# Kernel tuning notes

Hardware: AMD Instinct MI355X
Metric: run time of the kernel (lower is better)

## Reference

```python
import jax, jax.numpy as jnp
import numpy as np

NUM_EXPERTS = 32
TOP_K = 4
HIDDEN = 1024
FFN = 2048
BATCH, SEQ = 1, 1024


def setup_inputs() -> dict:
    key = jax.random.key(0)
    ks = jax.random.split(key, 4)
    s = 0.02
    return {
        "x": jax.random.normal(ks[0], (BATCH, SEQ, HIDDEN), jnp.float32),
        "gate_w": jax.random.normal(ks[1], (HIDDEN, NUM_EXPERTS), jnp.float32) * s,
        "gate_b": jnp.zeros((NUM_EXPERTS,), jnp.float32),
        "w1": jax.random.normal(ks[2], (NUM_EXPERTS, HIDDEN, FFN), jnp.float32) * s,
        "b1": jnp.zeros((NUM_EXPERTS, FFN), jnp.float32),
        "w2": jax.random.normal(ks[3], (NUM_EXPERTS, FFN, HIDDEN), jnp.float32) * s,
        "b2": jnp.zeros((NUM_EXPERTS, HIDDEN), jnp.float32),
        "load_ema": jnp.ones((NUM_EXPERTS,), jnp.float32) / NUM_EXPERTS,
        "top_k": TOP_K,
    }


def reference(x, gate_w, gate_b, w1, b1, w2, b2, load_ema, top_k):
    # x: [B, S, d]; eval-mode CompoundMoELayer forward.
    B, S, d = x.shape
    E = gate_w.shape[1]
    flat = x.reshape(-1, d)                              # [N, d]
    N = flat.shape[0]

    # --- router: gate logits -> top-k -> softmax over selected logits ---
    logits = flat @ gate_w + gate_b                      # [N, E]
    top_vals, top_idx = jax.lax.top_k(logits, top_k)     # [N, k]
    weights = jax.nn.softmax(top_vals, axis=-1)          # [N, k]

    # --- switch-style load-balance aux loss ---
    probs = jax.nn.softmax(logits, axis=-1)              # [N, E]
    counts = jax.nn.one_hot(top_idx, E, dtype=flat.dtype).sum(axis=1)  # [N, E]
    frac = counts.mean(axis=0) / top_k                   # [E] routed fraction
    base_aux = E * jnp.sum(frac * probs.mean(axis=0))

    # --- dense combine weights [N, E]: zero for non-selected experts ---
    comb = jnp.zeros((N, E), flat.dtype).at[jnp.arange(N)[:, None], top_idx].add(weights)

    # --- per-expert FFN (GELU, exact erf as torch default), combined ---
    def step(acc, p):
        W1, bb1, W2, bb2, ce = p                         # ce: [N] combine weight
        h = jax.nn.gelu(flat @ W1 + bb1, approximate=False)
        y = h @ W2 + bb2
        return acc + ce[:, None] * y, None

    out, _ = jax.lax.scan(step, jnp.zeros_like(flat), (w1, b1, w2, b2, comb.T))

    # --- compound entropy regularizer over expert load EMA buffer ---
    lp = load_ema / (load_ema.sum() + 1e-8)
    entropy = -jnp.sum(lp * jnp.log(lp + 1e-8))
    reg = jnp.log(jnp.asarray(E, flat.dtype)) - entropy
    aux = base_aux + 0.001 * reg
    return out.reshape(B, S, d), aux
```

## Files before the change

kernel.cpp:

```cpp
#include <hip/hip_runtime.h>
#include <hip/hip_bf16.h>
#include <cmath>

#define N_TOK 1024
#define DIM   1024
#define FFN   2048
#define NE    32
#define TOPK  4
#define TM    192
#define TN    64
#define BK    32
#define BS_STRIDE 40

typedef __attribute__((ext_vector_type(8))) short bf16x8;
typedef __attribute__((ext_vector_type(4))) float f32x4;

#define GLOBAL_AS __attribute__((address_space(1)))
#define LDS_AS    __attribute__((address_space(3)))

__device__ __forceinline__ void g2lds16(const void* g, void* l) {
    __builtin_amdgcn_global_load_lds((const GLOBAL_AS void*)g, (LDS_AS void*)l, 16, 0, 0);
}

__global__ __launch_bounds__(256) void router_kernel(
        const float* __restrict__ x, const float* __restrict__ gw,
        const float* __restrict__ gb, float* __restrict__ probs_mat,
        int* __restrict__ top_idx, float* __restrict__ top_w,
        __hip_bfloat16* __restrict__ xb) {
    __shared__ float part[8][32];
    __shared__ float logit_s[32];
    int t = threadIdx.x;
    int token = blockIdx.x;
    const float* xr = x + (size_t)token * DIM;
    {
        float4 v = *(const float4*)&xr[t * 4];
        union { __hip_bfloat16 h[4]; ushort4 u; } pk;
        pk.h[0] = __float2bfloat16(v.x); pk.h[1] = __float2bfloat16(v.y);
        pk.h[2] = __float2bfloat16(v.z); pk.h[3] = __float2bfloat16(v.w);
        *(ushort4*)&xb[(size_t)token * DIM + t * 4] = pk.u;
    }
    int e = t & 31, p = t >> 5;
    float acc = 0.f;
    int i0 = p * (DIM / 8);
    for (int i = 0; i < DIM / 8; ++i)
        acc += xr[i0 + i] * gw[(size_t)(i0 + i) * NE + e];
    part[p][e] = acc;
    __syncthreads();
    if (t < 64) {
        float l = -3e38f;
        if (t < 32) {
            l = gb[t];
            for (int q = 0; q < 8; ++q) l += part[q][t];
        }
        float m = l;
        for (int off = 32; off >= 1; off >>= 1) m = fmaxf(m, __shfl_xor(m, off, 64));
        float ex = (t < 32) ? expf(l - m) : 0.f;
        float den = ex;
        for (int off = 32; off >= 1; off >>= 1) den += __shfl_xor(den, off, 64);
        if (t < 32) probs_mat[(size_t)token * 32 + t] = ex / den;
        float v = l;
        float vals[TOPK]; int idxs[TOPK];
        for (int r = 0; r < TOPK; ++r) {
            float mv = v;
            for (int off = 32; off >= 1; off >>= 1) mv = fmaxf(mv, __shfl_xor(mv, off, 64));
            unsigned long long mask = __ballot(v == mv);
            int idx = __ffsll((unsigned long long)(mask & 0xffffffffull)) - 1;
            vals[r] = mv; idxs[r] = idx;
            if (t == idx) v = -3e38f;
        }
        if (t == 0) {
            float w[TOPK]; float ss = 0.f;
            for (int r = 0; r < TOPK; ++r) { w[r] = expf(vals[r] - vals[0]); ss += w[r]; }
            for (int r = 0; r < TOPK; ++r) {
                top_idx[token * TOPK + r] = idxs[r];
                top_w[token * TOPK + r] = w[r] / ss;
            }
        }
    }
}

__global__ void aux_kernel(const float* __restrict__ probs_mat, const int* __restrict__ top_idx,
                           const float* __restrict__ load_ema, int* __restrict__ offsets,
                           int* __restrict__ cursors, float* __restrict__ out_aux) {
    __shared__ int cnt_s[32];
    __shared__ float ps[32];
    __shared__ float psum_part[8][32];
    int t = threadIdx.x;
    if (t < 32) cnt_s[t] = 0;
    __syncthreads();
    for (int i = t; i < N_TOK * TOPK; i += 256) atomicAdd(&cnt_s[top_idx[i]], 1);
    int e = t & 31, p = t >> 5;
    float s = 0.f;
    for (int tok = p; tok < N_TOK; tok += 8) s += probs_mat[(size_t)tok * 32 + e];
    psum_part[p][e] = s;
    __syncthreads();
    if (t < 32) {
        float tot = 0.f;
        for (int q = 0; q < 8; ++q) tot += psum_part[q][t];
        ps[t] = tot;
    }
    __syncthreads();
    if (t == 0) {
        int off = 0;
        for (int i = 0; i < 32; ++i) { offsets[i] = off; cursors[i] = off; off += cnt_s[i]; }
        offsets[32] = off;
        float base = 0.f;
        for (int i = 0; i < 32; ++i) {
            float frac = (float)cnt_s[i] / (float)(N_TOK * TOPK);
            base += frac * (ps[i] / (float)N_TOK);
        }
        base *= (float)NE;
        float sum_ema = 0.f;
        for (int i = 0; i < 32; ++i) sum_ema += load_ema[i];
        float H = 0.f;
        for (int i = 0; i < 32; ++i) {
            float lp = load_ema[i] / (sum_ema + 1e-8f);
            H -= lp * logf(lp + 1e-8f);
        }
        *out_aux = base + 0.001f * (logf((float)NE) - H);
    }
}

__global__ void scatter_kernel(const int* __restrict__ top_idx, int* __restrict__ cursors,
                               int* __restrict__ pair_token, int* __restrict__ pair_of) {
    int token = blockIdx.x * 256 + threadIdx.x;
    if (token >= N_TOK) return;
    for (int s = 0; s < TOPK; ++s) {
        int e = top_idx[token * TOPK + s];
        int pos = atomicAdd(&cursors[e], 1);
        pair_token[pos] = token;
        pair_of[token * TOPK + s] = pos;
    }
}

__global__ __launch_bounds__(256, 4) void gemm1_kernel(
        const __hip_bfloat16* __restrict__ xb, const float* __restrict__ w1,
        const float* __restrict__ b1, const int* __restrict__ offsets,
        const int* __restrict__ pair_token, __hip_bfloat16* __restrict__ h) {
    int e = blockIdx.z;
    int m0 = offsets[e], Me = offsets[e + 1] - m0;
    int f0 = blockIdx.x * TN;

    __shared__ short As[4 * TM * 8];
    __shared__ __hip_bfloat16 Bs[TN * BS_STRIDE];
    __shared__ int toks[TM];

    int t = threadIdx.x;
    int w = t >> 6, ln = t & 63;
    int q = ln >> 4, lj = ln & 15;
    int bn = ln, bkb = w * 8;

    float bias[4];
#pragma unroll
    for (int ns = 0; ns < 4; ++ns) bias[ns] = b1[(size_t)e * FFN + f0 + ns * 16 + lj];

    for (int mb = 0; mb < Me; mb += TM) {
        int mlim = Me - mb; if (mlim > TM) mlim = TM;
        if (t < TM) {
            int r = t < mlim ? t : mlim - 1;
            toks[t] = pair_token[m0 + mb + r];
        }
        f32x4 acc[3][4] = {};
        for (int k0 = 0; k0 < DIM; k0 += BK) {
            __syncthreads();
#pragma unroll
            for (int c = 0; c < 3; ++c) {
                const __hip_bfloat16* src = xb + (size_t)toks[c * 64 + ln] * DIM + k0 + w * 8;
                g2lds16(src, As + (w * TM + c * 64) * 8);
            }
            {
                const float* bp = w1 + ((size_t)e * DIM + k0 + bkb) * FFN + f0 + bn;
                union { __hip_bfloat16 hb[8]; int4 v; } u;
#pragma unroll
                for (int j = 0; j < 8; ++j) u.hb[j] = __float2bfloat16(bp[(size_t)j * FFN]);
                *(int4*)&Bs[bn * BS_STRIDE + bkb] = u.v;
            }
            __syncthreads();
            bf16x8 af[3], bf[4];
#pragma unroll
            for (int ms = 0; ms < 3; ++ms)
                af[ms] = *(const bf16x8*)&As[(q * TM + w * 48 + ms * 16 + lj) * 8];
#pragma unroll
            for (int ns = 0; ns < 4; ++ns)
                bf[ns] = *(const bf16x8*)&Bs[(ns * 16 + lj) * BS_STRIDE + q * 8];
#pragma unroll
            for (int ms = 0; ms < 3; ++ms)
#pragma unroll
                for (int ns = 0; ns < 4; ++ns)
                    acc[ms][ns] = __builtin_amdgcn_mfma_f32_16x16x32_bf16(af[ms], bf[ns], acc[ms][ns], 0, 0, 0);
        }
#pragma unroll
        for (int ms = 0; ms < 3; ++ms) {
#pragma unroll
            for (int rr = 0; rr < 4; ++rr) {
                int rit = w * 48 + ms * 16 + q * 4 + rr;
                if (rit >= mlim) continue;
                size_t rowG = (size_t)(m0 + mb + rit);
#pragma unroll
                for (int ns = 0; ns < 4; ++ns) {
                    float v = acc[ms][ns][rr] + bias[ns];
                    float g = 0.5f * v * (1.f + erff(v * 0.70710678118654752f));
                    h[rowG * FFN + f0 + ns * 16 + lj] = __float2bfloat16(g);
                }
            }
        }
    }
}

__global__ __launch_bounds__(256, 4) void gemm2_kernel(
        const __hip_bfloat16* __restrict__ h, const float* __restrict__ w2,
        const int* __restrict__ offsets, float* __restrict__ y) {
    int e = blockIdx.z;
    int m0 = offsets[e], Me = offsets[e + 1] - m0;
    int d0 = blockIdx.x * TN;
    int kbase = blockIdx.y * (FFN / 2);
    float* yp = y + (size_t)blockIdx.y * N_TOK * TOPK * DIM;

    __shared__ short As[4 * TM * 8];
    __shared__ __hip_bfloat16 Bs[TN * BS_STRIDE];

    int t = threadIdx.x;
    int w = t >> 6, ln = t & 63;
    int q = ln >> 4, lj = ln & 15;
    int bn = ln, bkb = w * 8;

    for (int mb = 0; mb < Me; mb += TM) {
        int mlim = Me - mb; if (mlim > TM) mlim = TM;
        f32x4 acc[3][4] = {};
        for (int k0 = 0; k0 < FFN / 2; k0 += BK) {
            __syncthreads();
#pragma unroll
            for (int c = 0; c < 3; ++c) {
                int rit = c * 64 + ln;
                int r = rit < mlim ? rit : mlim - 1;
                const __hip_bfloat16* src = h + (size_t)(m0 + mb + r) * FFN + kbase + k0 + w * 8;
                g2lds16(src, As + (w * TM + c * 64) * 8);
            }
            {
                const float* bp = w2 + ((size_t)e * FFN + kbase + k0 + bkb) * DIM + d0 + bn;
                union { __hip_bfloat16 hb[8]; int4 v; } u;
#pragma unroll
                for (int j = 0; j < 8; ++j) u.hb[j] = __float2bfloat16(bp[(size_t)j * DIM]);
                *(int4*)&Bs[bn * BS_STRIDE + bkb] = u.v;
            }
            __syncthreads();
            bf16x8 af[3], bf[4];
#pragma unroll
            for (int ms = 0; ms < 3; ++ms)
                af[ms] = *(const bf16x8*)&As[(q * TM + w * 48 + ms * 16 + lj) * 8];
#pragma unroll
            for (int ns = 0; ns < 4; ++ns)
                bf[ns] = *(const bf16x8*)&Bs[(ns * 16 + lj) * BS_STRIDE + q * 8];
#pragma unroll
            for (int ms = 0; ms < 3; ++ms)
#pragma unroll
                for (int ns = 0; ns < 4; ++ns)
                    acc[ms][ns] = __builtin_amdgcn_mfma_f32_16x16x32_bf16(af[ms], bf[ns], acc[ms][ns], 0, 0, 0);
        }
#pragma unroll
        for (int ms = 0; ms < 3; ++ms) {
#pragma unroll
            for (int rr = 0; rr < 4; ++rr) {
                int rit = w * 48 + ms * 16 + q * 4 + rr;
                if (rit >= mlim) continue;
                size_t rowG = (size_t)(m0 + mb + rit);
#pragma unroll
                for (int ns = 0; ns < 4; ++ns)
                    yp[rowG * DIM + d0 + ns * 16 + lj] = acc[ms][ns][rr];
            }
        }
    }
}

__global__ void combine_kernel(const float* __restrict__ y, const float* __restrict__ b2,
        const int* __restrict__ top_idx, const float* __restrict__ top_w,
        const int* __restrict__ pair_of, float* __restrict__ out) {
    const float* y1 = y + (size_t)N_TOK * TOPK * DIM;
    int token = blockIdx.y;
    int j = blockIdx.x * 256 + threadIdx.x;
    float acc = 0.f;
#pragma unroll
    for (int s = 0; s < TOPK; ++s) {
        int e = top_idx[token * TOPK + s];
        float w = top_w[token * TOPK + s];
        int p = pair_of[token * TOPK + s];
        acc += w * (y[(size_t)p * DIM + j] + y1[(size_t)p * DIM + j] + b2[(size_t)e * DIM + j]);
    }
    out[(size_t)token * DIM + j] = acc;
}

extern "C" void kernel_launch(void* const* d_in, const int* in_sizes, int n_in,
                              void* d_out, int out_size, void* d_ws, size_t ws_size,
                              hipStream_t stream) {
    const float* x        = (const float*)d_in[0];
    const float* gate_w   = (const float*)d_in[1];
    const float* gate_b   = (const float*)d_in[2];
    const float* w1       = (const float*)d_in[3];
    const float* b1       = (const float*)d_in[4];
    const float* w2       = (const float*)d_in[5];
    const float* b2       = (const float*)d_in[6];
    const float* load_ema = (const float*)d_in[7];
    float* out = (float*)d_out;

    char* base = (char*)d_ws;
    size_t off = 0;
    auto alloc = [&](size_t bytes) {
        void* p = base + off;
        off = (off + bytes + 255) & ~(size_t)255;
        return p;
    };
    float* probs_mat = (float*)alloc(N_TOK * 32 * sizeof(float));
    int*   top_idx   = (int*)  alloc(N_TOK * TOPK * sizeof(int));
    float* top_w     = (float*)alloc(N_TOK * TOPK * sizeof(float));
    int*   offsets   = (int*)  alloc(33 * sizeof(int));
    int*   cursors   = (int*)  alloc(32 * sizeof(int));
    int*   pair_token= (int*)  alloc(N_TOK * TOPK * sizeof(int));
    int*   pair_of   = (int*)  alloc(N_TOK * TOPK * sizeof(int));
    __hip_bfloat16* xb = (__hip_bfloat16*)alloc((size_t)N_TOK * DIM * sizeof(__hip_bfloat16));
    __hip_bfloat16* h  = (__hip_bfloat16*)alloc((size_t)N_TOK * TOPK * FFN * sizeof(__hip_bfloat16));
    float* y         = (float*)alloc((size_t)2 * N_TOK * TOPK * DIM * sizeof(float));

    router_kernel<<<N_TOK, 256, 0, stream>>>(x, gate_w, gate_b, probs_mat, top_idx, top_w, xb);
    aux_kernel<<<1, 256, 0, stream>>>(probs_mat, top_idx, load_ema, offsets, cursors,
                                      out + (size_t)N_TOK * DIM);
    scatter_kernel<<<(N_TOK + 255) / 256, 256, 0, stream>>>(top_idx, cursors, pair_token, pair_of);
    {
        dim3 grid(FFN / TN, 1, NE);
        gemm1_kernel<<<grid, 256, 0, stream>>>(xb, w1, b1, offsets, pair_token, h);
    }
    {
        dim3 grid(DIM / TN, 2, NE);
        gemm2_kernel<<<grid, 256, 0, stream>>>(h, w2, offsets, y);
    }
    {
        dim3 grid(DIM / 256, N_TOK);
        combine_kernel<<<grid, 256, 0, stream>>>(y, b2, top_idx, top_w, pair_of, out);
    }
}
```

Baseline: 666.1 us.

## Double-buffer GEMM tiles and fuse weighted combine into gemm2 via atomics

Both expert GEMM kernels now double-buffer the LDS A/B tiles. The next K-slice's global loads and the bf16 conversion of the fp32 weights overlap the MFMA work on the current slice, and each iteration needs one barrier instead of two. The separate combine kernel and its large fp32 y intermediate are removed: gemm2 scales its partial results by the routing weight, adds the bias on the first K-half, and atomically accumulates straight into a pre-zeroed output. This cuts an 8M-float round trip through memory, at the cost of float atomic contention and an order-dependent, non-deterministic summation.

Result: no change. 676.4 us (+1.5%).

```diff
diff --git a/kernel.cpp b/kernel.cpp
--- a/kernel.cpp
+++ b/kernel.cpp
@@ -22,13 +22,16 @@
     __builtin_amdgcn_global_load_lds((const GLOBAL_AS void*)g, (LDS_AS void*)l, 16, 0, 0);
 }
 
+__global__ void zero_kernel(float4* __restrict__ p) {
+    p[blockIdx.x * 256 + threadIdx.x] = float4{0.f, 0.f, 0.f, 0.f};
+}
+
 __global__ __launch_bounds__(256) void router_kernel(
         const float* __restrict__ x, const float* __restrict__ gw,
         const float* __restrict__ gb, float* __restrict__ probs_mat,
         int* __restrict__ top_idx, float* __restrict__ top_w,
         __hip_bfloat16* __restrict__ xb) {
     __shared__ float part[8][32];
-    __shared__ float logit_s[32];
     int t = threadIdx.x;
     int token = blockIdx.x;
     const float* xr = x + (size_t)token * DIM;
@@ -121,15 +124,16 @@
     }
 }
 
-__global__ void scatter_kernel(const int* __restrict__ top_idx, int* __restrict__ cursors,
-                               int* __restrict__ pair_token, int* __restrict__ pair_of) {
+__global__ void scatter_kernel(const int* __restrict__ top_idx, const float* __restrict__ top_w,
+                               int* __restrict__ cursors,
+                               int* __restrict__ pair_token, float* __restrict__ pair_w) {
     int token = blockIdx.x * 256 + threadIdx.x;
     if (token >= N_TOK) return;
     for (int s = 0; s < TOPK; ++s) {
         int e = top_idx[token * TOPK + s];
         int pos = atomicAdd(&cursors[e], 1);
         pair_token[pos] = token;
-        pair_of[token * TOPK + s] = pos;
+        pair_w[pos] = top_w[token * TOPK + s];
     }
 }
 
@@ -139,10 +143,11 @@
         const int* __restrict__ pair_token, __hip_bfloat16* __restrict__ h) {
     int e = blockIdx.z;
     int m0 = offsets[e], Me = offsets[e + 1] - m0;
+    if (Me <= 0) return;
     int f0 = blockIdx.x * TN;
 
-    __shared__ short As[4 * TM * 8];
-    __shared__ __hip_bfloat16 Bs[TN * BS_STRIDE];
+    __shared__ __attribute__((aligned(16))) short As[2][4 * TM * 8];
+    __shared__ __attribute__((aligned(16))) __hip_bfloat16 Bs[2][TN * BS_STRIDE];
     __shared__ int toks[TM];
 
     int t = threadIdx.x;
@@ -154,40 +159,65 @@
 #pragma unroll
     for (int ns = 0; ns < 4; ++ns) bias[ns] = b1[(size_t)e * FFN + f0 + ns * 16 + lj];
 
+    const float* bbase = w1 + ((size_t)e * DIM + bkb) * FFN + f0 + bn;
+
     for (int mb = 0; mb < Me; mb += TM) {
         int mlim = Me - mb; if (mlim > TM) mlim = TM;
+        __syncthreads();
         if (t < TM) {
             int r = t < mlim ? t : mlim - 1;
             toks[t] = pair_token[m0 + mb + r];
         }
+        __syncthreads();
+
+        float br[8];
+#pragma unroll
+        for (int j = 0; j < 8; ++j) br[j] = bbase[(size_t)j * FFN];
+#pragma unroll
+        for (int c = 0; c < 3; ++c)
+            g2lds16(xb + (size_t)toks[c * 64 + ln] * DIM + w * 8,
+                    &As[0][(w * TM + c * 64) * 8]);
+        {
+            union { __hip_bfloat16 hb[8]; int4 v; } u;
+#pragma unroll
+            for (int j = 0; j < 8; ++j) u.hb[j] = __float2bfloat16(br[j]);
+            *(int4*)&Bs[0][bn * BS_STRIDE + bkb] = u.v;
+        }
+        __syncthreads();
+
         f32x4 acc[3][4] = {};
+        int cur = 0;
         for (int k0 = 0; k0 < DIM; k0 += BK) {
+            int nxt = cur ^ 1;
+            bool hasNext = (k0 + BK < DIM);
+            if (hasNext) {
+#pragma unroll
+                for (int j = 0; j < 8; ++j) br[j] = bbase[(size_t)(k0 + BK + j) * FFN];
+#pragma unroll
+                for (int c = 0; c < 3; ++c)
+                    g2lds16(xb + (size_t)toks[c * 64 + ln] * DIM + k0 + BK + w * 8,
+                            &As[nxt][(w * TM + c * 64) * 8]);
+            }
+            bf16x8 af[3], bfr[4];
+#pragma unroll
+            for (int ms = 0; ms < 3; ++ms)
+                af[ms] = *(const bf16x8*)&As[cur][(q * TM + w * 48 + ms * 16 + lj) * 8];
+#pragma unroll
+            for (int ns = 0; ns < 4; ++ns)
+                bfr[ns] = *(const bf16x8*)&Bs[cur][(ns * 16 + lj) * BS_STRIDE + q * 8];
+#pragma unroll
+            for (int ms = 0; ms < 3; ++ms)
+#pragma unroll
+                for (int ns = 0; ns < 4; ++ns)
+                    acc[ms][ns] = __builtin_amdgcn_mfma_f32_16x16x32_bf16(af[ms], bfr[ns], acc[ms][ns], 0, 0, 0);
+            if (hasNext) {
+                union { __hip_bfloat16 hb[8]; int4 v; } u;
+#pragma unroll
+                for (int j = 0; j < 8; ++j) u.hb[j] = __float2bfloat16(br[j]);
+                *(int4*)&Bs[nxt][bn * BS_STRIDE + bkb] = u.v;
+            }
             __syncthreads();
-#pragma unroll
-            for (int c = 0; c < 3; ++c) {
-                const __hip_bfloat16* src = xb + (size_t)toks[c * 64 + ln] * DIM + k0 + w * 8;
-                g2lds16(src, As + (w * TM + c * 64) * 8);
-            }
-            {
-                const float* bp = w1 + ((size_t)e * DIM + k0 + bkb) * FFN + f0 + bn;
-                union { __hip_bfloat16 hb[8]; int4 v; } u;
-#pragma unroll
-                for (int j = 0; j < 8; ++j) u.hb[j] = __float2bfloat16(bp[(size_t)j * FFN]);
-                *(int4*)&Bs[bn * BS_STRIDE + bkb] = u.v;
-            }
-            __syncthreads();
-            bf16x8 af[3], bf[4];
-#pragma unroll
-            for (int ms = 0; ms < 3; ++ms)
-                af[ms] = *(const bf16x8*)&As[(q * TM + w * 48 + ms * 16 + lj) * 8];
-#pragma unroll
-            for (int ns = 0; ns < 4; ++ns)
-                bf[ns] = *(const bf16x8*)&Bs[(ns * 16 + lj) * BS_STRIDE + q * 8];
-#pragma unroll
-            for (int ms = 0; ms < 3; ++ms)
-#pragma unroll
-                for (int ns = 0; ns < 4; ++ns)
-                    acc[ms][ns] = __builtin_amdgcn_mfma_f32_16x16x32_bf16(af[ms], bf[ns], acc[ms][ns], 0, 0, 0);
+            cur = nxt;
         }
 #pragma unroll
         for (int ms = 0; ms < 3; ++ms) {
@@ -209,53 +239,88 @@
 
 __global__ __launch_bounds__(256, 4) void gemm2_kernel(
         const __hip_bfloat16* __restrict__ h, const float* __restrict__ w2,
-        const int* __restrict__ offsets, float* __restrict__ y) {
+        const float* __restrict__ b2, const int* __restrict__ offsets,
+        const int* __restrict__ pair_token, const float* __restrict__ pair_w,
+        float* __restrict__ out) {
     int e = blockIdx.z;
     int m0 = offsets[e], Me = offsets[e + 1] - m0;
+    if (Me <= 0) return;
     int d0 = blockIdx.x * TN;
     int kbase = blockIdx.y * (FFN / 2);
-    float* yp = y + (size_t)blockIdx.y * N_TOK * TOPK * DIM;
-
-    __shared__ short As[4 * TM * 8];
-    __shared__ __hip_bfloat16 Bs[TN * BS_STRIDE];
+
+    __shared__ __attribute__((aligned(16))) short As[2][4 * TM * 8];
+    __shared__ __attribute__((aligned(16))) __hip_bfloat16 Bs[2][TN * BS_STRIDE];
 
     int t = threadIdx.x;
     int w = t >> 6, ln = t & 63;
     int q = ln >> 4, lj = ln & 15;
     int bn = ln, bkb = w * 8;
 
+    float bias[4];
+#pragma unroll
+    for (int ns = 0; ns < 4; ++ns)
+        bias[ns] = (blockIdx.y == 0) ? b2[(size_t)e * DIM + d0 + ns * 16 + lj] : 0.f;
+
+    const float* bbase = w2 + ((size_t)e * FFN + kbase + bkb) * DIM + d0 + bn;
+
     for (int mb = 0; mb < Me; mb += TM) {
         int mlim = Me - mb; if (mlim > TM) mlim = TM;
+        __syncthreads();
+
+        float br[8];
+#pragma unroll
+        for (int j = 0; j < 8; ++j) br[j] = bbase[(size_t)j * DIM];
+#pragma unroll
+        for (int c = 0; c < 3; ++c) {
+            int rit = c * 64 + ln;
+            int r = rit < mlim ? rit : mlim - 1;
+            g2lds16(h + (size_t)(m0 + mb + r) * FFN + kbase + w * 8,
+                    &As[0][(w * TM + c * 64) * 8]);
+        }
+        {
+            union { __hip_bfloat16 hb[8]; int4 v; } u;
+#pragma unroll
+            for (int j = 0; j < 8; ++j) u.hb[j] = __float2bfloat16(br[j]);
+            *(int4*)&Bs[0][bn * BS_STRIDE + bkb] = u.v;
+        }
+        __syncthreads();
+
         f32x4 acc[3][4] = {};
+        int cur = 0;
         for (int k0 = 0; k0 < FFN / 2; k0 += BK) {
+            int nxt = cur ^ 1;
+            bool hasNext = (k0 + BK < FFN / 2);
+            if (hasNext) {
+#pragma unroll
+                for (int j = 0; j < 8; ++j) br[j] = bbase[(size_t)(k0 + BK + j) * DIM];
+#pragma unroll
+                for (int c = 0; c < 3; ++c) {
+                    int rit = c * 64 + ln;
+                    int r = rit < mlim ? rit : mlim - 1;
+                    g2lds16(h + (size_t)(m0 + mb + r) * FFN + kbase + k0 + BK + w * 8,
+                            &As[nxt][(w * TM + c * 64) * 8]);
+                }
+            }
+            bf16x8 af[3], bfr[4];
+#pragma unroll
+            for (int ms = 0; ms < 3; ++ms)
+                af[ms] = *(const bf16x8*)&As[cur][(q * TM + w * 48 + ms * 16 + lj) * 8];
+#pragma unroll
+            for (int ns = 0; ns < 4; ++ns)
+                bfr[ns] = *(const bf16x8*)&Bs[cur][(ns * 16 + lj) * BS_STRIDE + q * 8];
+#pragma unroll
+            for (int ms = 0; ms < 3; ++ms)
+#pragma unroll
+                for (int ns = 0; ns < 4; ++ns)
+                    acc[ms][ns] = __builtin_amdgcn_mfma_f32_16x16x32_bf16(af[ms], bfr[ns], acc[ms][ns], 0, 0, 0);
+            if (hasNext) {
+                union { __hip_bfloat16 hb[8]; int4 v; } u;
+#pragma unroll
+                for (int j = 0; j < 8; ++j) u.hb[j] = __float2bfloat16(br[j]);
+                *(int4*)&Bs[nxt][bn * BS_STRIDE + bkb] = u.v;
+            }
             __syncthreads();
-#pragma unroll
-            for (int c = 0; c < 3; ++c) {
-                int rit = c * 64 + ln;
-                int r = rit < mlim ? rit : mlim - 1;
-                const __hip_bfloat16* src = h + (size_t)(m0 + mb + r) * FFN + kbase + k0 + w * 8;
-                g2lds16(src, As + (w * TM + c * 64) * 8);
-            }
-            {
-                const float* bp = w2 + ((size_t)e * FFN + kbase + k0 + bkb) * DIM + d0 + bn;
-                union { __hip_bfloat16 hb[8]; int4 v; } u;
-#pragma unroll
-                for (int j = 0; j < 8; ++j) u.hb[j] = __float2bfloat16(bp[(size_t)j * DIM]);
-                *(int4*)&Bs[bn * BS_STRIDE + bkb] = u.v;
-            }
-            __syncthreads();
-            bf16x8 af[3], bf[4];
-#pragma unroll
-            for (int ms = 0; ms < 3; ++ms)
-                af[ms] = *(const bf16x8*)&As[(q * TM + w * 48 + ms * 16 + lj) * 8];
-#pragma unroll
-            for (int ns = 0; ns < 4; ++ns)
-                bf[ns] = *(const bf16x8*)&Bs[(ns * 16 + lj) * BS_STRIDE + q * 8];
-#pragma unroll
-            for (int ms = 0; ms < 3; ++ms)
-#pragma unroll
-                for (int ns = 0; ns < 4; ++ns)
-                    acc[ms][ns] = __builtin_amdgcn_mfma_f32_16x16x32_bf16(af[ms], bf[ns], acc[ms][ns], 0, 0, 0);
+            cur = nxt;
         }
 #pragma unroll
         for (int ms = 0; ms < 3; ++ms) {
@@ -263,30 +328,16 @@
             for (int rr = 0; rr < 4; ++rr) {
                 int rit = w * 48 + ms * 16 + q * 4 + rr;
                 if (rit >= mlim) continue;
-                size_t rowG = (size_t)(m0 + mb + rit);
+                int pr = m0 + mb + rit;
+                int tok = pair_token[pr];
+                float wgt = pair_w[pr];
 #pragma unroll
                 for (int ns = 0; ns < 4; ++ns)
-                    yp[rowG * DIM + d0 + ns * 16 + lj] = acc[ms][ns][rr];
-            }
-        }
-    }
-}
-
-__global__ void combine_kernel(const float* __restrict__ y, const float* __restrict__ b2,
-        const int* __restrict__ top_idx, const float* __restrict__ top_w,
-        const int* __restrict__ pair_of, float* __restrict__ out) {
-    const float* y1 = y + (size_t)N_TOK * TOPK * DIM;
-    int token = blockIdx.y;
-    int j = blockIdx.x * 256 + threadIdx.x;
-    float acc = 0.f;
-#pragma unroll
-    for (int s = 0; s < TOPK; ++s) {
-        int e = top_idx[token * TOPK + s];
-        float w = top_w[token * TOPK + s];
-        int p = pair_of[token * TOPK + s];
-        acc += w * (y[(size_t)p * DIM + j] + y1[(size_t)p * DIM + j] + b2[(size_t)e * DIM + j]);
-    }
-    out[(size_t)token * DIM + j] = acc;
+                    atomicAdd(&out[(size_t)tok * DIM + d0 + ns * 16 + lj],
+                              wgt * (acc[ms][ns][rr] + bias[ns]));
+            }
+        }
+    }
 }
 
 extern "C" void kernel_launch(void* const* d_in, const int* in_sizes, int n_in,
@@ -315,25 +366,22 @@
     int*   offsets   = (int*)  alloc(33 * sizeof(int));
     int*   cursors   = (int*)  alloc(32 * sizeof(int));
     int*   pair_token= (int*)  alloc(N_TOK * TOPK * sizeof(int));
-    int*   pair_of   = (int*)  alloc(N_TOK * TOPK * sizeof(int));
+    float* pair_w    = (float*)alloc(N_TOK * TOPK * sizeof(float));
     __hip_bfloat16* xb = (__hip_bfloat16*)alloc((size_t)N_TOK * DIM * sizeof(__hip_bfloat16));
     __hip_bfloat16* h  = (__hip_bfloat16*)alloc((size_t)N_TOK * TOPK * FFN * sizeof(__hip_bfloat16));
-    float* y         = (float*)alloc((size_t)2 * N_TOK * TOPK * DIM * sizeof(float));
-
+
+    zero_kernel<<<N_TOK * DIM / (256 * 4), 256, 0, stream>>>((float4*)out);
     router_kernel<<<N_TOK, 256, 0, stream>>>(x, gate_w, gate_b, probs_mat, top_idx, top_w, xb);
     aux_kernel<<<1, 256, 0, stream>>>(probs_mat, top_idx, load_ema, offsets, cursors,
                                       out + (size_t)N_TOK * DIM);
-    scatter_kernel<<<(N_TOK + 255) / 256, 256, 0, stream>>>(top_idx, cursors, pair_token, pair_of);
+    scatter_kernel<<<(N_TOK + 255) / 256, 256, 0, stream>>>(top_idx, top_w, cursors,
+                                                            pair_token, pair_w);
     {
         dim3 grid(FFN / TN, 1, NE);
         gemm1_kernel<<<grid, 256, 0, stream>>>(xb, w1, b1, offsets, pair_token, h);
     }
     {
         dim3 grid(DIM / TN, 2, NE);
-        gemm2_kernel<<<grid, 256, 0, stream>>>(h, w2, offsets, y);
-    }
-    {
-        dim3 grid(DIM / 256, N_TOK);
-        combine_kernel<<<grid, 256, 0, stream>>>(y, b2, top_idx, top_w, pair_of, out);
-    }
-}
+        gemm2_kernel<<<grid, 256, 0, stream>>>(h, w2, b2, offsets, pair_token, pair_w, out);
+    }
+}
```
